# Performance work log

Hardware: AMD Instinct MI355X
Metric: run time of the kernel (lower is better)

The kernel has to match this reference:

```python
import jax, jax.numpy as jnp
import numpy as np

B, A, C, L, NH, SCALE = 1, 5, 64, 4, 8, 2
H = W = 24
S = 2 * C
KS = 5


def layernorm(x, g, b, eps=1e-5):
    m = x.mean(-1, keepdims=True)
    v = ((x - m) ** 2).mean(-1, keepdims=True)
    return (x - m) * jax.lax.rsqrt(v + eps) * g + b


def pe_1d(n, d):
    # PositionEncoding: temperature**(2*(i//2)/d), sin of even cols then cos of odd cols
    g = jnp.arange(d, dtype=jnp.float32)
    g = 10000.0 ** (2.0 * jnp.floor(g / 2.0) / d)
    p = jnp.arange(n, dtype=jnp.float32)[:, None] / g[None, :]
    return jnp.concatenate([jnp.sin(p[:, 0::2]), jnp.cos(p[:, 1::2])], axis=1)  # [n, d]


def mha(qk, v, in_w, out_w, nh, mask=None):
    # qk, v: [Lq, Bt, D]; torch nn.MultiheadAttention, bias-free, q=k=qk, value=v
    Lq, Bt, D = qk.shape
    dh = D // nh
    wq, wk, wv = jnp.split(in_w, 3, axis=0)
    q = (qk @ wq.T).reshape(Lq, Bt, nh, dh)
    k = (qk @ wk.T).reshape(Lq, Bt, nh, dh)
    vv = (v @ wv.T).reshape(Lq, Bt, nh, dh)
    s = jnp.einsum('lbhd,mbhd->bhlm', q, k) / jnp.sqrt(jnp.float32(dh))
    if mask is not None:
        s = s + mask
    a = jax.nn.softmax(s, axis=-1)
    o = jnp.einsum('bhlm,mbhd->lbhd', a, vv).reshape(Lq, Bt, D)
    return o @ out_w.T


def unfold3x3(x):
    # F.unfold(k=3, pad=1).permute(2,0,1): [N,c,h,w] -> [h*w, N, 9c] (c, kh, kw ordering)
    N, c, h, w = x.shape
    xp = jnp.pad(x, ((0, 0), (0, 0), (1, 1), (1, 1)))
    p = jnp.stack([xp[:, :, i:i + h, j:j + w] for i in range(3) for j in range(3)], axis=2)
    return p.reshape(N, c * 9, h * w).transpose(2, 0, 1)


def conv_hw(x5, w):
    # Conv3d kernel (1,3,3) pad (0,1,1): 2D conv per angular view
    Bc, Ci, Aa, h, w_ = x5.shape
    y = jax.lax.conv_general_dilated(
        x5.transpose(0, 2, 1, 3, 4).reshape(Bc * Aa, Ci, h, w_), w, (1, 1), ((1, 1), (1, 1)),
        dimension_numbers=('NCHW', 'OIHW', 'NCHW'))
    return y.reshape(Bc, Aa, w.shape[0], h, w_).transpose(0, 2, 1, 3, 4)


def window_mask(h, w, k):
    # SpaTrans.gen_mask: additive -inf outside a k x k local window
    kl, kr = k // 2, k - k // 2
    i = jnp.arange(h)
    j = jnp.arange(w)
    mh = (i[None, :] >= i[:, None] - kl) & (i[None, :] < i[:, None] + kr)
    mw = (j[None, :] >= j[:, None] - kl) & (j[None, :] < j[:, None] + kr)
    m = (mh[:, None, :, None] & mw[None, :, None, :]).reshape(h * w, h * w)
    return jnp.where(m, 0.0, -jnp.inf).astype(jnp.float32)


def setup_inputs() -> dict:
    key = jax.random.key(0)
    ks = iter(jax.random.split(key, 64))
    def nrm(shape, s=0.02):
        return jax.random.normal(next(ks), shape, dtype=jnp.float32) * s
    d = {}
    d['lr'] = jax.random.normal(next(ks), (B, 1, A * H, A * W), dtype=jnp.float32)
    Hh, Wh = H * SCALE, W * SCALE
    ch = -1.0 + (2.0 * jnp.arange(Hh, dtype=jnp.float32) + 1.0) / Hh
    cw = -1.0 + (2.0 * jnp.arange(Wh, dtype=jnp.float32) + 1.0) / Wh
    g = jnp.stack(jnp.meshgrid(ch, cw, indexing='ij'), axis=-1).reshape(-1, 2)
    d['coord'] = jnp.broadcast_to(g, (B, Hh * Wh, 2))
    d['conv0_w'] = nrm((C, 1, 3, 3), 0.1)
    d['convi_w'] = nrm((3, C, C, 3, 3), 0.05)
    d['ang_ln_g'] = jnp.ones((L, C)); d['ang_ln_b'] = jnp.zeros((L, C))
    d['ang_in'] = nrm((L, 3 * C, C)); d['ang_out'] = nrm((L, C, C))
    d['ang_ff_g'] = jnp.ones((L, C)); d['ang_ff_b'] = jnp.zeros((L, C))
    d['ang_w1'] = nrm((L, 2 * C, C)); d['ang_w2'] = nrm((L, C, 2 * C))
    d['spa_mlp'] = nrm((L, S, 9 * C))
    d['spa_ln_g'] = jnp.ones((L, S)); d['spa_ln_b'] = jnp.zeros((L, S))
    d['spa_in'] = nrm((L, 3 * S, S)); d['spa_out'] = nrm((L, S, S))
    d['spa_ff_g'] = jnp.ones((L, S)); d['spa_ff_b'] = jnp.zeros((L, S))
    d['spa_w1'] = nrm((L, 2 * S, S)); d['spa_w2'] = nrm((L, S, 2 * S))
    d['spa_lin'] = nrm((L, C, S))
    IN = A * A * C + 2 + 2 * A * A
    d['imp_w0'] = nrm((320, IN)); d['imp_b0'] = jnp.zeros((320,))
    d['imp_w1'] = nrm((320, 320)); d['imp_b1'] = jnp.zeros((320,))
    d['imp_w2'] = nrm((3 * A * A, 320)); d['imp_b2'] = jnp.zeros((3 * A * A,))
    return d


def reference(lr, coord, conv0_w, convi_w, ang_ln_g, ang_ln_b, ang_in, ang_out,
              ang_ff_g, ang_ff_b, ang_w1, ang_w2, spa_mlp, spa_ln_g, spa_ln_b,
              spa_in, spa_out, spa_ff_g, spa_ff_b, spa_w1, spa_w2, spa_lin,
              imp_w0, imp_b0, imp_w1, imp_b1, imp_w2, imp_b2):
    Bn = lr.shape[0]
    # 'b c (a1 h) (a2 w) -> b c (a1 a2) h w'
    x = lr.reshape(Bn, 1, A, H, A, W).transpose(0, 1, 2, 4, 3, 5).reshape(Bn, 1, A * A, H, W)
    spa_pe_img = ((pe_1d(H, C)[:, None, :] + pe_1d(W, C)[None, :, :]) * 0.5).transpose(2, 0, 1)[None]  # [1,C,h,w]
    ang_pe = pe_1d(A * A, C)[:, None, :]  # [A^2,1,C]
    buf = conv_hw(x, conv0_w)
    t = buf
    for i in range(3):
        t = jax.nn.leaky_relu(conv_hw(t, convi_w[i]), 0.2)
    buf = t + buf
    mask = window_mask(H, W, KS)
    blk = buf
    for l in range(L):
        # ---- AngTrans: tokens [A^2, B*h*w, C]
        tok = blk.transpose(2, 0, 3, 4, 1).reshape(A * A, Bn * H * W, C)
        tn = layernorm(tok + ang_pe, ang_ln_g[l], ang_ln_b[l])
        tok = mha(tn, tok, ang_in[l], ang_out[l], NH) + tok
        ff = layernorm(tok, ang_ff_g[l], ang_ff_b[l])
        tok = jax.nn.relu(ff @ ang_w1[l].T) @ ang_w2[l].T + tok
        blk = tok.reshape(A * A, Bn, H, W, C).transpose(1, 4, 0, 2, 3)
        # ---- SpaTrans: tokens [h*w, B*A^2, 2C] with local-window mask
        xb = blk.transpose(0, 2, 1, 3, 4).reshape(Bn * A * A, C, H, W)
        tok = unfold3x3(xb) @ spa_mlp[l].T
        pe_tok = unfold3x3(spa_pe_img) @ spa_mlp[l].T
        tn = layernorm(tok + pe_tok, spa_ln_g[l], spa_ln_b[l])
        tok = mha(tn, tok, spa_in[l], spa_out[l], NH, mask) + tok
        ff = layernorm(tok, spa_ff_g[l], spa_ff_b[l])
        tok = jax.nn.relu(ff @ spa_w1[l].T) @ spa_w2[l].T + tok
        t5 = tok.reshape(H, W, Bn, A * A, S).transpose(2, 4, 3, 0, 1)  # b s a h w
        blk = jnp.einsum('os,bsahw->boahw', spa_lin[l], t5)  # 1x1x1 Conv3d
    buf = blk + buf
    # 'b c (a1 a2) h w -> b c (a1 h) (a2 w)'
    feat_lr = buf.reshape(Bn, C, A, A, H, W).transpose(0, 1, 2, 4, 3, 5).reshape(Bn, C, A * H, A * W)
    Hh, Wh = H * SCALE, W * SCALE
    # per-view bilinear upsample (align_corners=False)
    v = feat_lr.reshape(Bn, C, A, H, A, W).transpose(0, 2, 4, 1, 3, 5).reshape(Bn * A * A, C, H, W)
    v = jax.image.resize(v, (Bn * A * A, C, Hh, Wh), method='bilinear')
    feat_hr = v.reshape(Bn, A, A, C, Hh, Wh).transpose(0, 4, 5, 1, 2, 3).reshape(Bn, Hh, Wh, A * A * C)
    # nearest grid_sample of LR cell-center coords -> relative coord
    c_ = jnp.clip(coord + 1e-6, -1 + 1e-6, 1 - 1e-6)
    ih = jnp.clip(jnp.round(((c_[..., 0] + 1) * H - 1) / 2), 0, H - 1)
    iw = jnp.clip(jnp.round(((c_[..., 1] + 1) * W - 1) / 2), 0, W - 1)
    qh = -1.0 + (2.0 * ih + 1.0) / H
    qw = -1.0 + (2.0 * iw + 1.0) / W
    rel = jnp.stack([(coord[..., 0] - qh) * H, (coord[..., 1] - qw) * W], axis=-1).reshape(Bn, Hh, Wh, 2)
    au = 0.5 + jnp.arange(A, dtype=jnp.float32)  # make_coord ranges [0,A]
    ca = jnp.stack(jnp.meshgrid(au, au, indexing='ij'), axis=-1).reshape(-1)
    ca = jnp.broadcast_to(ca, (Bn, Hh, Wh, 2 * A * A))
    inp = jnp.concatenate([feat_hr, rel, ca], axis=-1)
    h0 = jax.nn.relu(inp @ imp_w0.T + imp_b0)
    h1 = jax.nn.relu(h0 @ imp_w1.T + imp_b1)
    o = h1 @ imp_w2.T + imp_b2
    # 'b h w (a1 a2 c) -> b c (a1 h) (a2 w)', c=3
    return o.reshape(Bn, Hh, Wh, A, A, 3).transpose(0, 5, 3, 1, 4, 2).reshape(Bn, 3, A * Hh, A * Wh)
```

## Files before the change

### kernel.cpp

```cpp
#include <hip/hip_runtime.h>
#include <math.h>

typedef short  s16x4 __attribute__((ext_vector_type(4)));
typedef short  s16x8 __attribute__((ext_vector_type(8)));
typedef float  f32x4 __attribute__((ext_vector_type(4)));

static const size_t PE25_  = 0;
static const size_t SPAPE_ = 2048;
static const size_t X_     = 38912;
static const size_t CAV_   = 53312;
static const size_t PETOK_ = 54272;
static const size_t W9C_   = 349184;
static const size_t W9S_   = 459776;
static const size_t BUF_   = 754688;
static const size_t BLK_   = 1676288;
static const size_t ATOK_  = 2597888;
static const size_t TNF_   = 3519488;
static const size_t STOK_  = 4441088;
static const size_t STOK2_ = 6284288;
static const size_t AO_    = 8127488;
static const size_t QKV_   = 9970688;
static const size_t WS_FLOATS = 15500288;
static const size_t T0_ = QKV_ + 2764800;
static const size_t T1_ = T0_ + 921600;
// ... 57 lines not shown
    #pragma unroll
    for (int i = 0; i < 2; ++i) {
      const char* pa = ldsA + (((wr*2 + i)*2 + ks) << 11) + (lane << 4);
      ah[i] = *(const s16x8*)pa;
      al[i] = *(const s16x8*)(pa + 1024);
      const char* pb = ldsB + (((wc*2 + i)*2 + ks) << 11) + (lane << 4);
      bh[i] = *(const s16x8*)pb;
      bl[i] = *(const s16x8*)(pb + 1024);
    }
    #pragma unroll
    for (int i = 0; i < 2; ++i) {
      #pragma unroll
      for (int j = 0; j < 2; ++j) {
        acc[i][j] = __builtin_amdgcn_mfma_f32_16x16x32_bf16(ah[i], bh[j], acc[i][j], 0, 0, 0);
        acc[i][j] = __builtin_amdgcn_mfma_f32_16x16x32_bf16(ah[i], bl[j], acc[i][j], 0, 0, 0);
        acc[i][j] = __builtin_amdgcn_mfma_f32_16x16x32_bf16(al[i], bh[j], acc[i][j], 0, 0, 0);
      }
    }
  }
}

__device__ inline void epilogue(f32x4 acc[2][2], const float* bias, const float* res,
                                float* out, int N, int m0, int n0,
                                int wr, int wc, int lane, int act) {
  int colb = n0 + wc*32 + (lane & 15);
  int rowb = m0 + wr*32 + ((lane >> 4) << 2);
  #pragma unroll
  for (int j = 0; j < 2; ++j) {
    int cc = colb + j*16;
    if (cc >= N) continue;
    float bv = bias ? bias[cc] : 0.f;
    #pragma unroll
    for (int i = 0; i < 2; ++i) {
      #pragma unroll
      for (int r = 0; r < 4; ++r) {
        int rr = rowb + i*16 + r;
        float v = acc[i][j][r] + bv;
        if (act == 1) v = fmaxf(v, 0.f);
        else if (act == 2) v = v > 0.f ? v : 0.2f*v;
        if (res) v += res[(long)rr*N + cc];
        if (act == 3) {
          int hh = rr / 48, ww2 = rr % 48, q = cc / 3, ch = cc % 3;
          out[ch*57600 + ((q/5)*48 + hh)*240 + (q%5)*48 + ww2] = v;
        } else if (act == 4) {
          ((ushort*)out)[(long)rr*N + cc] = f2bf(v);
        } else {
          out[(long)rr*N + cc] = v;
        }
      }
    }
  }
}

template<int K, int LN>
__global__ __launch_bounds__(256) void mgemm3_k(
    const float* __restrict__ A, const float* __restrict__ A2, int nsplit,
    const float* __restrict__ pe, int pe_mode,
    const float* __restrict__ g, const float* __restrict__ bb,
    const float* __restrict__ W, const float* __restrict__ bias,
    const float* __restrict__ res, float* __restrict__ out,
    int N, int act, int Mreal, int Mpad) {
  constexpr int NCH = K / 64;
  __shared__ char Apl[NCH * 16384];
  __shared__ char Bp[16384];
  __shared__ float sw_[4][64][2];
  __shared__ float sf_[64][2];
  int bid = blockIdx.x;
  int m = bid % Mpad, nt = bid / Mpad;
  if (m >= Mreal) return;
  int m0 = m*64, n0 = nt*64;
  int t = threadIdx.x, lane = t & 63, wave = t >> 6;
  int wr = wave >> 1, wc = wave & 1;
  bool use_norm = LN && (n0 < nsplit);

  if (LN && use_norm) {
    f32x4 rv[NCH][4];
    float sA[4], sQ[4];
    #pragma unroll
    for (int i = 0; i < 4; ++i) { sA[i] = 0.f; sQ[i] = 0.f; }
    #pragma unroll
    for (int ch = 0; ch < NCH; ++ch)
      #pragma unroll
      for (int i = 0; i < 4; ++i) {
        int row, kof, wo; slot_decode(i, wave, lane, row, kof, wo);
        int gk = ch*64 + kof;
        f32x4 av = *(const f32x4*)&A[(long)(m0 + row)*K + gk];
        if (pe_mode == 0)      av += *(const f32x4*)&pe[(long)(m0/576)*K + gk];
        else if (pe_mode == 1) av += *(const f32x4*)&pe[(long)(m0%576 + row)*K + gk];
        rv[ch][i] = av;
        #pragma unroll
        for (int e = 0; e < 4; ++e) { sA[i] += av[e]; sQ[i] = fmaf(av[e], av[e], sQ[i]); }
      }
    #pragma unroll
    for (int i = 0; i < 4; ++i) {
      float s = sA[i], q = sQ[i];
      s += __shfl_xor(s, 1, 64);  q += __shfl_xor(q, 1, 64);
      s += __shfl_xor(s, 32, 64); q += __shfl_xor(q, 32, 64);
      if ((lane & 1) == 0 && lane < 32) {
        int row = i*16 + (lane >> 1);
        sw_[wave][row][0] = s; sw_[wave][row][1] = q;
      }
    }
    __syncthreads();
    if (t < 64) {
      float s = sw_[0][t][0] + sw_[1][t][0] + sw_[2][t][0] + sw_[3][t][0];
      float q = sw_[0][t][1] + sw_[1][t][1] + sw_[2][t][1] + sw_[3][t][1];
      float mean = s / K, var = q / K - mean*mean;
      sf_[t][0] = mean; sf_[t][1] = rsqrtf(var + 1e-5f);
    }
    __syncthreads();
    #pragma unroll
    for (int ch = 0; ch < NCH; ++ch)
      #pragma unroll
      for (int i = 0; i < 4; ++i) {
        int row, kof, wo; slot_decode(i, wave, lane, row, kof, wo);
        int gk = ch*64 + kof;
        float mean = sf_[row][0], rstd = sf_[row][1];
        f32x4 gv = *(const f32x4*)&g[gk];
        f32x4 bv = *(const f32x4*)&bb[gk];
        f32x4 nv;
        #pragma unroll
        for (int e = 0; e < 4; ++e) nv[e] = (rv[ch][i][e] - mean)*rstd*gv[e] + bv[e];
        store_split(Apl + ch*16384 + wo, nv);
      }
  } else {
    const float* As = LN ? A2 : A;
    #pragma unroll
    for (int ch = 0; ch < NCH; ++ch)
      #pragma unroll
      for (int i = 0; i < 4; ++i) {
        int row, kof, wo; slot_decode(i, wave, lane, row, kof, wo);
        f32x4 av = *(const f32x4*)&As[(long)(m0 + row)*K + ch*64 + kof];
        store_split(Apl + ch*16384 + wo, av);
      }
  }

  f32x4 pb[4];
  #pragma unroll
  for (int i = 0; i < 4; ++i) {
    int row, kof, wo; slot_decode(i, wave, lane, row, kof, wo);
    int br = n0 + row;
    pb[i] = (br < N) ? *(const f32x4*)&W[(long)br*K + kof] : (f32x4){0.f,0.f,0.f,0.f};
  }
  __syncthreads();
  f32x4 acc[2][2];
  #pragma unroll
  for (int i = 0; i < 2; ++i)
    #pragma unroll
    for (int j = 0; j < 2; ++j) acc[i][j] = (f32x4){0.f,0.f,0.f,0.f};
  for (int ch = 0; ch < NCH; ++ch) {
    #pragma unroll
    for (int i = 0; i < 4; ++i) {
      int row, kof, wo; slot_decode(i, wave, lane, row, kof, wo);
      store_split(Bp + wo, pb[i]);
    }
    __syncthreads();
    if (ch + 1 < NCH) {
      #pragma unroll
      for (int i = 0; i < 4; ++i) {
        int row, kof, wo; slot_decode(i, wave, lane, row, kof, wo);
        int br = n0 + row;
        pb[i] = (br < N) ? *(const f32x4*)&W[(long)br*K + (ch+1)*64 + kof]
                         : (f32x4){0.f,0.f,0.f,0.f};
      }
    }
    mfma_step(Apl + ch*16384, Bp, lane, wr, wc, acc);
    if (ch + 1 < NCH) __syncthreads();
  }
  epilogue(acc, bias, res, out, N, m0, n0, wr, wc, lane, act);
}

__global__ __launch_bounds__(256) void cgemm3_k(
    const float* __restrict__ in, const float* __restrict__ W9, long wstride,
    const float* __restrict__ res, float* __restrict__ out, long ostride,
    int N, int act, int Mreal, int Mpad) {
  __shared__ float halo[144 * 68];
  __shared__ char Ap[16384], Bp[16384];
  int bid = blockIdx.x;
  int m = bid % Mpad, nt = bid / Mpad;
  if (m >= Mreal) return;
  int ly = blockIdx.y;
  W9  += (long)ly * wstride;
  out += (long)ly * ostride;
  int m0 = m*64, n0 = nt*64;
  int a = m0 / 576, off = m0 % 576;
  int h_lo = off/24 - 1, h_hi = (off + 63)/24 + 1;
  int RH = h_hi - h_lo + 1;
  int t = threadIdx.x, lane = t & 63, wave = t >> 6;
  int wr = wave >> 1, wc = wave & 1;
  for (int sidx = t; sidx < RH*24*16; sidx += 256) {
    int tokr = sidx >> 4, c4 = (sidx & 15) << 2;
    int h = h_lo + tokr/24, w = tokr % 24;
    f32x4 v = {0.f,0.f,0.f,0.f};
    if ((unsigned)h < 24u) v = *(const f32x4*)&in[(long)(a*576 + h*24 + w)*64 + c4];
    *(f32x4*)&halo[tokr*68 + c4] = v;
  }
  f32x4 pb[4];
  #pragma unroll
  for (int i = 0; i < 4; ++i) {
    int row, kof, wo; slot_decode(i, wave, lane, row, kof, wo);
    int br = n0 + row;
    pb[i] = (br < N) ? *(const f32x4*)&W9[(long)br*64 + kof] : (f32x4){0.f,0.f,0.f,0.f};
  }
  __syncthreads();
  f32x4 acc[2][2];
  #pragma unroll
  for (int i = 0; i < 2; ++i)
    #pragma unroll
    for (int j = 0; j < 2; ++j) acc[i][j] = (f32x4){0.f,0.f,0.f,0.f};
  for (int ij = 0; ij < 9; ++ij) {
    int di = ij/3 - 1, dj = ij%3 - 1;
    #pragma unroll
    for (int i = 0; i < 4; ++i) {
      int row, kof, wo; slot_decode(i, wave, lane, row, kof, wo);
      int tok = off + row;
      int h2 = tok/24 + di, w2 = tok%24 + dj;
      f32x4 v = {0.f,0.f,0.f,0.f};
      if ((unsigned)h2 < 24u && (unsigned)w2 < 24u)
        v = *(const f32x4*)&halo[((h2 - h_lo)*24 + w2)*68 + kof];
      store_split(Ap + wo, v);
      store_split(Bp + wo, pb[i]);
    }
    __syncthreads();
    if (ij < 8) {
      #pragma unroll
      for (int i = 0; i < 4; ++i) {
        int row, kof, wo; slot_decode(i, wave, lane, row, kof, wo);
        int br = n0 + row;
        pb[i] = (br < N) ? *(const f32x4*)&W9[((long)(ij+1)*N + br)*64 + kof]
                         : (f32x4){0.f,0.f,0.f,0.f};
      }
    }
    mfma_step(Ap, Bp, lane, wr, wc, acc);
    if (ij < 8) __syncthreads();
  }
  epilogue(acc, nullptr, res, out, N, m0, n0, wr, wc, lane, act);
}

__global__ __launch_bounds__(256) void ang_mega_k(
    const ushort* __restrict__ qkv, const float* __restrict__ Wout,
    const float* __restrict__ blkr, const float* __restrict__ g,
    const float* __restrict__ bb, float* __restrict__ atok, float* __restrict__ tnf) {
  int hw = blockIdx.x;
  __shared__ float lq[25*192];
  __shared__ float lao[25*64];
  __shared__ float po[25*68];
  __shared__ float wout[64*65];
  __shared__ float st[25][2];
  int t = threadIdx.x;
  for (int idx = t; idx < 600; idx += 256) {
    int a3 = idx / 24, c8 = (idx % 24) * 8;
    s16x8 r = *(const s16x8*)&qkv[(long)(a3*576 + hw)*192 + c8];
    #pragma unroll
    for (int e = 0; e < 8; ++e) lq[a3*192 + c8 + e] = bf2f((ushort)r[e]);
  }
  for (int idx = t; idx < 4096; idx += 256) {
    int c = idx >> 6, d = idx & 63;
    wout[c*65 + d] = Wout[idx];
  }
  __syncthreads();
  if (t < 200) {
    int l = t / 8, head = t & 7;
    const float* q = lq + l*192 + head*8;
    float s[25]; float mx = -1e30f;
    #pragma unroll
    for (int mm = 0; mm < 25; ++mm) {
      const float* kk = lq + mm*192 + 64 + head*8;
      float acc = 0.f;
      #pragma unroll
      for (int d = 0; d < 8; ++d) acc = fmaf(q[d], kk[d], acc);
      acc *= 0.3535533905932738f;
      s[mm] = acc; mx = fmaxf(mx, acc);
    }
    float sum = 0.f;
    #pragma unroll
    for (int mm = 0; mm < 25; ++mm) { s[mm] = expf(s[mm] - mx); sum += s[mm]; }
    float inv = 1.f / sum;
    #pragma unroll
    for (int d = 0; d < 8; ++d) {
      float acc = 0.f;
      #pragma unroll
      for (int mm = 0; mm < 25; ++mm) acc = fmaf(s[mm], lq[mm*192 + 128 + head*8 + d], acc);
      lao[l*64 + head*8 + d] = acc * inv;
    }
  }
  __syncthreads();
  for (int idx = t; idx < 1600; idx += 256) {
    int tok = idx >> 6, c = idx & 63;
    const float* ar = &lao[tok*64];
    const float* wr = &wout[c*65];
    float accp = 0.f;
    #pragma unroll 16
    for (int d = 0; d < 64; ++d) accp = fmaf(ar[d], wr[d], accp);
    po[tok*68 + c] = accp + blkr[(long)(tok*576 + hw)*64 + c];
  }
  __syncthreads();
  if (t < 25) {
    float s = 0.f, q = 0.f;
    for (int c = 0; c < 64; ++c) { float x = po[t*68 + c]; s += x; q = fmaf(x, x, q); }
    float mean = s / 64.f, var = q / 64.f - mean*mean;
    st[t][0] = mean; st[t][1] = rsqrtf(var + 1e-5f);
  }
  __syncthreads();
  for (int idx = t; idx < 1600; idx += 256) {
    int tok = idx >> 6, c = idx & 63;
    float x = po[tok*68 + c];
    long gidx = (long)(tok*576 + hw)*64 + c;
    atok[gidx] = x;
    tnf[gidx] = (x - st[tok][0]) * st[tok][1] * g[c] + bb[c];
  }
}

__global__ __launch_bounds__(256) void ffn_ang_k(
    const float* __restrict__ tnf, const float* __restrict__ w1,
    const float* __restrict__ w2, float* __restrict__ atok,
    int Mreal, int Mpad) {
  __shared__ char Ap[16384], Bp[16384], Hp[2][16384];
  int bid = blockIdx.x;
  int m = bid % Mpad;
  if (m >= Mreal) return;
  int m0 = m*64;
  int t = threadIdx.x, lane = t & 63, wave = t >> 6;
  int wr = wave >> 1, wc = wave & 1;
  #pragma unroll
  for (int i = 0; i < 4; ++i) {
    int row, kof, wo; slot_decode(i, wave, lane, row, kof, wo);
    f32x4 av = *(const f32x4*)&tnf[(long)(m0 + row)*64 + kof];
    store_split(Ap + wo, av);
  }
  f32x4 pb[4];
  #pragma unroll
  for (int i = 0; i < 4; ++i) {
    int row, kof, wo; slot_decode(i, wave, lane, row, kof, wo);
    pb[i] = *(const f32x4*)&w1[(long)row*64 + kof];
  }
  __syncthreads();
  for (int nt = 0; nt < 2; ++nt) {
    #pragma unroll
    for (int i = 0; i < 4; ++i) {
      int row, kof, wo; slot_decode(i, wave, lane, row, kof, wo);
      store_split(Bp + wo, pb[i]);
    }
    __syncthreads();
    #pragma unroll
    for (int i = 0; i < 4; ++i) {
      int row, kof, wo; slot_decode(i, wave, lane, row, kof, wo);
      pb[i] = (nt == 0) ? *(const f32x4*)&w1[(long)(64 + row)*64 + kof]
                        : *(const f32x4*)&w2[(long)row*128 + kof];
    }
    f32x4 acc[2][2];
    #pragma unroll
    for (int i = 0; i < 2; ++i)
      #pragma unroll
      for (int j = 0; j < 2; ++j) acc[i][j] = (f32x4){0.f,0.f,0.f,0.f};
    mfma_step(Ap, Bp, lane, wr, wc, acc);
    #pragma unroll
    for (int jj = 0; jj < 2; ++jj)
      #pragma unroll
      for (int ii = 0; ii < 2; ++ii)
        #pragma unroll
        for (int r = 0; r < 4; ++r) {
          int rr = wr*32 + ii*16 + ((lane >> 4) << 2) + r;
          int cc = wc*32 + jj*16 + (lane & 15);
          scatter_split(Hp[nt], rr, cc, fmaxf(acc[ii][jj][r], 0.f));
        }
    __syncthreads();
  }
  f32x4 acc2[2][2];
  #pragma unroll
  for (int i = 0; i < 2; ++i)
    #pragma unroll
    for (int j = 0; j < 2; ++j) acc2[i][j] = (f32x4){0.f,0.f,0.f,0.f};
  for (int ch = 0; ch < 2; ++ch) {
    #pragma unroll
    for (int i = 0; i < 4; ++i) {
      int row, kof, wo; slot_decode(i, wave, lane, row, kof, wo);
      store_split(Bp + wo, pb[i]);
    }
    __syncthreads();
    if (ch == 0) {
      #pragma unroll
      for (int i = 0; i < 4; ++i) {
        int row, kof, wo; slot_decode(i, wave, lane, row, kof, wo);
        pb[i] = *(const f32x4*)&w2[(long)row*128 + 64 + kof];
      }
    }
    mfma_step(Hp[ch], Bp, lane, wr, wc, acc2);
    if (ch == 0) __syncthreads();
  }
  epilogue(acc2, nullptr, atok, atok, 64, m0, 0, wr, wc, lane, 0);
}

__global__ __launch_bounds__(256) void megaspa_k(
    const ushort* __restrict__ qkv, const float* __restrict__ stok,
    const float* __restrict__ wout, const float* __restrict__ g,
    const float* __restrict__ bb, const float* __restrict__ w1,
    const float* __restrict__ w2, const float* __restrict__ wlin,
    float* __restrict__ outb, int Mreal, int Mpad) {
  __shared__ char Aop[32768];
  __shared__ char Bp[16384];
  __shared__ char Hp[4][16384];
  __shared__ float Yf[64][132];
  __shared__ float st[64][2];
  int bid = blockIdx.x;
  int m = bid % Mpad;
  if (m >= Mreal) return;
  int m0 = m*64;
  int t = threadIdx.x, lane = t & 63, wave = t >> 6;
  int wr = wave >> 1, wc = wave & 1;
  float* HpF = (float*)Hp;

  for (int idx = t; idx < 2048; idx += 256) {
    *(f32x4*)&HpF[idx*4] =
        *(const f32x4*)&stok[(long)(m0 + (idx >> 5))*128 + ((idx & 31) << 2)];
  }

  #pragma unroll
  for (int task = 0; task < 2; ++task) {
    int tid = t + task*256;
    int rr = tid >> 3, head = tid & 7;
    int x = m0 + rr;
    int hw = x % 576, h = hw / 24, w = hw % 24;
    float qr[16];
    ld_bf16x16(qkv + (long)x*384 + head*16, qr);
    float s[25]; float mx = -1e30f;
    #pragma unroll
    for (int ro = 0; ro < 5; ++ro) {
      int h2 = h + ro - 2;
      s16x8 k0[5], k1[5];
      #pragma unroll
      for (int co = 0; co < 5; ++co) {
        int xt = x + (ro - 2)*24 + (co - 2);
        xt = min(max(xt, 0), 14399);
        const ushort* kp = qkv + (long)xt*384 + 128 + head*16;
        k0[co] = *(const s16x8*)kp;
        k1[co] = *(const s16x8*)(kp + 8);
      }
      #pragma unroll
      for (int co = 0; co < 5; ++co) {
        int w2 = w + co - 2;
        float sc = -1e30f;
        if (h2 >= 0 && h2 < 24 && w2 >= 0 && w2 < 24) {
          sc = 0.f;
          #pragma unroll
          for (int d = 0; d < 8; ++d) sc = fmaf(qr[d], bf2f((ushort)k0[co][d]), sc);
          #pragma unroll
          for (int d = 0; d < 8; ++d) sc = fmaf(qr[8+d], bf2f((ushort)k1[co][d]), sc);
          sc *= 0.25f;
        }
        s[ro*5 + co] = sc; mx = fmaxf(mx, sc);
      }
    }
    float sum = 0.f;
    #pragma unroll
    for (int i = 0; i < 25; ++i) {
      float e = (s[i] > -1e29f) ? expf(s[i] - mx) : 0.f;
      s[i] = e; sum += e;
    }
    float inv = 1.f / sum;
    float acc[16];
    #pragma unroll
    for (int d = 0; d < 16; ++d) acc[d] = 0.f;
    #pragma unroll
    for (int ro = 0; ro < 5; ++ro) {
      s16x8 v0[5], v1[5];
      #pragma unroll
      for (int co = 0; co < 5; ++co) {
        int xt = x + (ro - 2)*24 + (co - 2);
        xt = min(max(xt, 0), 14399);
        const ushort* vp = qkv + (long)xt*384 + 256 + head*16;
        v0[co] = *(const s16x8*)vp;
        v1[co] = *(const s16x8*)(vp + 8);
      }
      #pragma unroll
      for (int co = 0; co < 5; ++co) {
        float sv = s[ro*5 + co];
        #pragma unroll
        for (int d = 0; d < 8; ++d) acc[d] = fmaf(sv, bf2f((ushort)v0[co][d]), acc[d]);
        #pragma unroll
        for (int d = 0; d < 8; ++d) acc[8+d] = fmaf(sv, bf2f((ushort)v1[co][d]), acc[8+d]);
      }
    }
    #pragma unroll
    for (int d = 0; d < 16; ++d) {
      int cc = head*16 + d;
      scatter_split(Aop + (cc >> 6)*16384, rr, cc & 63, acc[d] * inv);
    }
  }

  for (int nt = 0; nt < 2; ++nt) {
    f32x4 acc[2][2];
    #pragma unroll
    for (int i = 0; i < 2; ++i)
      #pragma unroll
      for (int j = 0; j < 2; ++j) acc[i][j] = (f32x4){0.f,0.f,0.f,0.f};
    for (int ch = 0; ch < 2; ++ch) {
      __syncthreads();
      #pragma unroll
      for (int i = 0; i < 4; ++i) {
        int row, kof, wo; slot_decode(i, wave, lane, row, kof, wo);
        f32x4 bv = *(const f32x4*)&wout[(long)(nt*64 + row)*128 + ch*64 + kof];
        store_split(Bp + wo, bv);
      }
      __syncthreads();
      mfma_step(Aop + ch*16384, Bp, lane, wr, wc, acc);
    }
    int colb = nt*64 + wc*32 + (lane & 15);
    int rowb = wr*32 + ((lane >> 4) << 2);
    #pragma unroll
    for (int j = 0; j < 2; ++j)
      #pragma unroll
      for (int i = 0; i < 2; ++i)
        #pragma unroll
        for (int r = 0; r < 4; ++r) {
          int rr = rowb + i*16 + r, cc = colb + j*16;
          Yf[rr][cc] = acc[i][j][r] + HpF[rr*128 + cc];
        }
  }
  __syncthreads();

  {
    int row = t >> 2, q4 = t & 3;
    const float* yr = &Yf[row][q4*32];
    float s = 0.f, sq = 0.f;
    #pragma unroll
    for (int j2 = 0; j2 < 32; ++j2) { float xv = yr[j2]; s += xv; sq = fmaf(xv, xv, sq); }
    s += __shfl_xor(s, 1, 64); sq += __shfl_xor(sq, 1, 64);
    s += __shfl_xor(s, 2, 64); sq += __shfl_xor(sq, 2, 64);
    if (q4 == 0) {
      float mean = s / 128.f, var = sq / 128.f - mean*mean;
      st[row][0] = mean; st[row][1] = rsqrtf(var + 1e-5f);
    }
  }
  __syncthreads();
  #pragma unroll
  for (int ch = 0; ch < 2; ++ch)
    #pragma unroll
    for (int i = 0; i < 4; ++i) {
      int row, kof, wo; slot_decode(i, wave, lane, row, kof, wo);
      int gk = ch*64 + kof;
      f32x4 xv = *(const f32x4*)&Yf[row][gk];
      float mean = st[row][0], rstd = st[row][1];
      f32x4 gv = *(const f32x4*)&g[gk];
      f32x4 bv = *(const f32x4*)&bb[gk];
      f32x4 nv;
      #pragma unroll
      for (int e = 0; e < 4; ++e) nv[e] = (xv[e] - mean)*rstd*gv[e] + bv[e];
      store_split(Aop + ch*16384 + wo, nv);
    }

  for (int nt = 0; nt < 4; ++nt) {
    f32x4 acc[2][2];
    #pragma unroll
    for (int i = 0; i < 2; ++i)
      #pragma unroll
      for (int j = 0; j < 2; ++j) acc[i][j] = (f32x4){0.f,0.f,0.f,0.f};
    for (int ch = 0; ch < 2; ++ch) {
      __syncthreads();
      #pragma unroll
      for (int i = 0; i < 4; ++i) {
        int row, kof, wo; slot_decode(i, wave, lane, row, kof, wo);
        f32x4 bv = *(const f32x4*)&w1[(long)(nt*64 + row)*128 + ch*64 + kof];
        store_split(Bp + wo, bv);
      }
      __syncthreads();
      mfma_step(Aop + ch*16384, Bp, lane, wr, wc, acc);
    }
    #pragma unroll
    for (int jj = 0; jj < 2; ++jj)
      #pragma unroll
      for (int ii = 0; ii < 2; ++ii)
        #pragma unroll
        for (int r = 0; r < 4; ++r) {
          int rr = wr*32 + ii*16 + ((lane >> 4) << 2) + r;
          int cc = wc*32 + jj*16 + (lane & 15);
          scatter_split(Hp[nt], rr, cc, fmaxf(acc[ii][jj][r], 0.f));
        }
  }

  for (int nt2 = 0; nt2 < 2; ++nt2) {
    f32x4 acc2[2][2];
    #pragma unroll
    for (int i = 0; i < 2; ++i)
      #pragma unroll
      for (int j = 0; j < 2; ++j) acc2[i][j] = (f32x4){0.f,0.f,0.f,0.f};
    for (int ch = 0; ch < 4; ++ch) {
      __syncthreads();
      #pragma unroll
      for (int i = 0; i < 4; ++i) {
        int row, kof, wo; slot_decode(i, wave, lane, row, kof, wo);
        f32x4 bv = *(const f32x4*)&w2[(long)(nt2*64 + row)*256 + ch*64 + kof];
        store_split(Bp + wo, bv);
      }
      __syncthreads();
      mfma_step(Hp[ch], Bp, lane, wr, wc, acc2);
    }
    #pragma unroll
    for (int jj = 0; jj < 2; ++jj)
      #pragma unroll
      for (int ii = 0; ii < 2; ++ii)
        #pragma unroll
        for (int r = 0; r < 4; ++r) {
          int rr = wr*32 + ii*16 + ((lane >> 4) << 2) + r;
          int cc = wc*32 + jj*16 + (lane & 15);
          scatter_split(Aop + nt2*16384, rr, cc,
                        acc2[ii][jj][r] + Yf[rr][nt2*64 + cc]);
        }
  }

  f32x4 acc3[2][2];
  #pragma unroll
  for (int i = 0; i < 2; ++i)
    #pragma unroll
    for (int j = 0; j < 2; ++j) acc3[i][j] = (f32x4){0.f,0.f,0.f,0.f};
  for (int ch = 0; ch < 2; ++ch) {
    __syncthreads();
    #pragma unroll
    for (int i = 0; i < 4; ++i) {
      int row, kof, wo; slot_decode(i, wave, lane, row, kof, wo);
      f32x4 bv = *(const f32x4*)&wlin[(long)row*128 + ch*64 + kof];
      store_split(Bp + wo, bv);
    }
    __syncthreads();
    mfma_step(Aop + ch*16384, Bp, lane, wr, wc, acc3);
  }
  epilogue(acc3, nullptr, nullptr, outb, 64, m0, 0, wr, wc, lane, 0);
}

__global__ __launch_bounds__(256) void zgemm3_k(
    const float* __restrict__ buf, const float* __restrict__ blk,
    const float* __restrict__ W0, float* __restrict__ Zp) {
  __shared__ char Ap[16384], Bp[16384];
  int bid = blockIdx.x;
  int m = bid % 16; if (m >= 9) return;
  int nz = bid / 16;
  int n = nz % 5, z = nz / 5;
  int m0 = m*64, n0 = n*64;
  int t = threadIdx.x, lane = t & 63, wave = t >> 6;
  int wr = wave >> 1, wc = wave & 1;
  f32x4 pa[4], pb[4];
  #pragma unroll
  for (int i = 0; i < 4; ++i) {
    int row, kof, wo; slot_decode(i, wave, lane, row, kof, wo);
    long tok = (long)(z*5)*576 + m0 + row;
    pa[i] = *(const f32x4*)&buf[tok*64 + kof];
    pa[i] += *(const f32x4*)&blk[tok*64 + kof];
    pb[i] = *(const f32x4*)&W0[(long)(n0 + row)*1652 + (z*5)*64 + kof];
  }
  f32x4 acc[2][2];
  #pragma unroll
  for (int i = 0; i < 2; ++i)
    #pragma unroll
    for (int j = 0; j < 2; ++j) acc[i][j] = (f32x4){0.f,0.f,0.f,0.f};
  for (int q = 0; q < 5; ++q) {
    #pragma unroll
    for (int i = 0; i < 4; ++i) {
      int row, kof, wo; slot_decode(i, wave, lane, row, kof, wo);
      store_split(Ap + wo, pa[i]);
      store_split(Bp + wo, pb[i]);
    }
    __syncthreads();
    if (q < 4) {
      #pragma unroll
      for (int i = 0; i < 4; ++i) {
        int row, kof, wo; slot_decode(i, wave, lane, row, kof, wo);
        long tok = (long)(z*5 + q + 1)*576 + m0 + row;
        pa[i] = *(const f32x4*)&buf[tok*64 + kof];
        pa[i] += *(const f32x4*)&blk[tok*64 + kof];
        pb[i] = *(const f32x4*)&W0[(long)(n0 + row)*1652 + (z*5 + q + 1)*64 + kof];
      }
    }
    mfma_step(Ap, Bp, lane, wr, wc, acc);
    if (q < 4) __syncthreads();
  }
  epilogue(acc, nullptr, nullptr, Zp + (long)z*184320, 320, m0, n0, wr, wc, lane, 0);
}

__global__ void combine_k(const float* __restrict__ Zp, const float* __restrict__ cav,
                          const float* __restrict__ coord, float* __restrict__ h0out) {
  int gidx = blockIdx.x * 256 + threadIdx.x;
  if (gidx >= 2304 * 320) return;
  int p = gidx / 320, o = gidx % 320;
  int hh = p / 48, ww = p % 48;
  float sh = hh * 0.5f - 0.25f, sw = ww * 0.5f - 0.25f;
  int h0i = (int)floorf(sh); float fh = sh - h0i;
  int w0i = (int)floorf(sw); float fw = sw - w0i;
  int h0c = max(h0i, 0), h1c = min(h0i + 1, 23);
  int w0c = max(w0i, 0), w1c = min(w0i + 1, 23);
  int i00 = (h0c*24 + w0c)*320 + o, i01 = (h0c*24 + w1c)*320 + o;
  int i10 = (h1c*24 + w0c)*320 + o, i11 = (h1c*24 + w1c)*320 + o;
  float z00 = 0.f, z01 = 0.f, z10 = 0.f, z11 = 0.f;
  #pragma unroll
  for (int z = 0; z < 5; ++z) {
    const float* Zz = Zp + (long)z*184320;
    z00 += Zz[i00]; z01 += Zz[i01]; z10 += Zz[i10]; z11 += Zz[i11];
  }
  float v = (1.f-fh)*((1.f-fw)*z00 + fw*z01) + fh*((1.f-fw)*z10 + fw*z11);
  #pragma unroll
  for (int d = 0; d < 2; ++d) {
    float co = coord[p*2 + d];
    float cc = fminf(fmaxf(co + 1e-6f, -1.f + 1e-6f), 1.f - 1e-6f);
    float ix = rintf(((cc + 1.f)*24.f - 1.f)*0.5f);
    ix = fminf(fmaxf(ix, 0.f), 23.f);
    float q = -1.f + (2.f*ix + 1.f)/24.f;
    v = fmaf((co - q)*24.f, cav[320*(d+1) + o], v);
  }
  h0out[gidx] = fmaxf(v + cav[o], 0.f);
}

__device__ inline float pe_val(int pos, int c) {
  int j = c & 31;
  float freq = powf(10000.f, -2.f * (float)j / 64.f);
  float arg = (float)pos * freq;
  return (c < 32) ? sinf(arg) : cosf(arg);
}

__global__ void setup_k(const float* __restrict__ lr, const float* __restrict__ convi_w,
                        const float* __restrict__ spa_mlp,
                        const float* __restrict__ imp_w0, const float* __restrict__ imp_b0,
                        float* pe25, float* spa_pe, float* X, float* w9c, float* w9s,
                        float* cav) {
  int g = blockIdx.x * 256 + threadIdx.x;
  if (g < 1600) { pe25[g] = pe_val(g >> 6, g & 63); return; }
  g -= 1600;
  if (g < 36864) {
    int hw = g >> 6, c = g & 63; int h = hw / 24, w = hw % 24;
    spa_pe[g] = 0.5f * (pe_val(h, c) + pe_val(w, c)); return;
  }
  g -= 36864;
  if (g < 14400) {
    int aa = g / 576, hw = g % 576, h = hw / 24, w = hw % 24;
    X[g] = lr[((aa/5)*24 + h)*120 + (aa%5)*24 + w]; return;
  }
  g -= 14400;
  if (g < 110592) {
    int cv = g / 36864, rem = g % 36864;
    int ij = rem / 4096, oc = rem % 4096;
    int o = oc >> 6, c = oc & 63;
    w9c[g] = convi_w[((long)(cv*64 + o)*64 + c)*9 + ij]; return;
  }
  g -= 110592;
  if (g < 294912) {
    int l = g / 73728, rem = g % 73728;
    int ij = rem / 8192, oc = rem % 8192;
    int o = oc >> 6, c = oc & 63;
    w9s[g] = spa_mlp[((long)(l*128 + o))*576 + c*9 + ij]; return;
  }
  g -= 294912;
// ... 29 lines not shown
  float wv[9];
  #pragma unroll
  for (int q = 0; q < 9; ++q) wv[q] = W[lane*9 + q];
  #pragma unroll
  for (int p = 0; p < 12; ++p) {
    float acc = 0.f;
    #pragma unroll
    for (int i = 0; i < 3; ++i)
      #pragma unroll
      for (int j = 0; j < 3; ++j)
        acc = fmaf(patch[sp][i][p + j], wv[i*3 + j], acc);
    out[(long)(a*576 + h*24 + w0 + p)*64 + lane] = acc;
  }
}

extern "C" void kernel_launch(void* const* d_in, const int* in_sizes, int n_in,
                              void* d_out, int out_size, void* d_ws, size_t ws_size,
                              hipStream_t stream) {
  (void)in_sizes; (void)n_in; (void)out_size;
  if (ws_size < (size_t)WS_FLOATS * 4) return;
  float* ws = (float*)d_ws;

  const float* lr       = (const float*)d_in[0];
  const float* coord    = (const float*)d_in[1];
  const float* conv0_w  = (const float*)d_in[2];
  const float* convi_w  = (const float*)d_in[3];
  const float* ang_ln_g = (const float*)d_in[4];
  const float* ang_ln_b = (const float*)d_in[5];
  const float* ang_in   = (const float*)d_in[6];
  const float* ang_out  = (const float*)d_in[7];
  const float* ang_ff_g = (const float*)d_in[8];
  const float* ang_ff_b = (const float*)d_in[9];
  const float* ang_w1   = (const float*)d_in[10];
  const float* ang_w2   = (const float*)d_in[11];
  const float* spa_mlp  = (const float*)d_in[12];
  const float* spa_ln_g = (const float*)d_in[13];
  const float* spa_ln_b = (const float*)d_in[14];
  const float* spa_in   = (const float*)d_in[15];
  const float* spa_out  = (const float*)d_in[16];
  const float* spa_ff_g = (const float*)d_in[17];
  const float* spa_ff_b = (const float*)d_in[18];
  const float* spa_w1   = (const float*)d_in[19];
  const float* spa_w2   = (const float*)d_in[20];
  const float* spa_lin  = (const float*)d_in[21];
  const float* imp_w0   = (const float*)d_in[22];
  const float* imp_b0   = (const float*)d_in[23];
  const float* imp_w1   = (const float*)d_in[24];
  const float* imp_b1   = (const float*)d_in[25];
  const float* imp_w2   = (const float*)d_in[26];
  const float* imp_b2   = (const float*)d_in[27];

  float* pe25 = ws + PE25_;  float* spa_pe = ws + SPAPE_;  float* X = ws + X_;
  float* cav = ws + CAV_;    float* petok = ws + PETOK_;
  float* w9c = ws + W9C_;    float* w9s = ws + W9S_;
  float* buf = ws + BUF_;    float* blk = ws + BLK_;      float* atok = ws + ATOK_;
  float* tnf = ws + TNF_;    float* stok = ws + STOK_;
  float* qkvf = ws + QKV_;   ushort* qkvh = (ushort*)(ws + QKV_);
  float* t0 = ws + T0_;      float* t1 = ws + T1_;
  float* Zp = ws + ZP_;      float* h0 = ws + H0_;        float* h1 = ws + H1_;

  setup_k<<<1792, 256, 0, stream>>>(lr, convi_w, spa_mlp, imp_w0, imp_b0,
                                    pe25, spa_pe, X, w9c, w9s, cav);
  conv0_k<<<300, 256, 0, stream>>>(X, conv0_w, buf);
  cgemm3_k<<<dim3(232,1), 256, 0, stream>>>(buf, w9c,         0, nullptr, t0,  0, 64, 2, 225, 232);
  cgemm3_k<<<dim3(232,1), 256, 0, stream>>>(t0,  w9c + 36864, 0, nullptr, t1,  0, 64, 2, 225, 232);
  cgemm3_k<<<dim3(232,1), 256, 0, stream>>>(t1,  w9c + 73728, 0, buf,     buf, 0, 64, 2, 225, 232);
  cgemm3_k<<<dim3(32, 4), 256, 0, stream>>>(spa_pe, w9s, 73728, nullptr, petok, 73728,
                                            128, 0, 9, 16);

  for (int l = 0; l < 4; ++l) {
    const float* blkr = (l == 0) ? buf : blk;
    mgemm3_k<64,1><<<696, 256, 0, stream>>>(blkr, blkr, 128, pe25, 0,
        ang_ln_g + l*64, ang_ln_b + l*64, ang_in + l*192*64, nullptr, nullptr,
        qkvf, 192, 4, 225, 232);
    ang_mega_k<<<576, 256, 0, stream>>>(qkvh, ang_out + l*64*64, blkr,
        ang_ff_g + l*64, ang_ff_b + l*64, atok, tnf);
    ffn_ang_k<<<232, 256, 0, stream>>>(tnf, ang_w1 + l*128*64, ang_w2 + l*64*128,
        atok, 225, 232);
    cgemm3_k<<<dim3(464,1), 256, 0, stream>>>(atok, w9s + l*73728, 0, nullptr, stok, 0,
        128, 0, 225, 232);
    mgemm3_k<128,1><<<1392, 256, 0, stream>>>(stok, stok, 256, petok + l*73728, 1,
        spa_ln_g + l*128, spa_ln_b + l*128, spa_in + l*384*128, nullptr, nullptr,
        qkvf, 384, 4, 225, 232);
    megaspa_k<<<232, 256, 0, stream>>>(qkvh, stok, spa_out + l*128*128,
        spa_ff_g + l*128, spa_ff_b + l*128, spa_w1 + l*256*128, spa_w2 + l*128*256,
        spa_lin + l*64*128, blk, 225, 232);
  }

  zgemm3_k<<<400, 256, 0, stream>>>(buf, blk, imp_w0, Zp);
  combine_k<<<2880, 256, 0, stream>>>(Zp, cav, coord, h0);
  mgemm3_k<320,0><<<200, 256, 0, stream>>>(h0, h0, 0, nullptr, -1, nullptr, nullptr,
      imp_w1, imp_b1, nullptr, h1, 320, 1, 36, 40);
  mgemm3_k<320,0><<<80, 256, 0, stream>>>(h1, h1, 0, nullptr, -1, nullptr, nullptr,
      imp_w2, imp_b2, nullptr, (float*)d_out, 75, 3, 36, 40);
}
```

Baseline: 652.4 us.

## Split megaspa kernel across two 256-thread wave groups at 512 threads

The fused spatial-attention/FFN kernel now launches with 512 threads, and its two wave groups each take one 64-column output tile of the out-projection, FFN and norm stages, with double-buffered B and hidden tiles. Shared memory is reorganised: the residual is kept in a single Rf buffer that is accumulated in place, and the FFN hidden layer is computed in two rounds of two 64-wide tiles instead of four stored tiles. This doubles the waves per block to raise parallelism, since only 225 blocks run. In exchange, the final linear projection runs on only half the waves, and the extra threads raise per-block register and LDS pressure. Elsewhere only whitespace changes.

```diff
diff --git a/kernel.cpp b/kernel.cpp
--- a/kernel.cpp
+++ b/kernel.cpp
@@ -163,7 +163,8 @@
     for (int ch = 0; ch < NCH; ++ch)
       #pragma unroll
       for (int i = 0; i < 4; ++i) {
-        int row, kof, wo; slot_decode(i, wave, lane, row, kof, wo);
+        int row, kof, wo;
+        slot_decode(i, wave, lane, row, kof, wo);
         int gk = ch*64 + kof;
         f32x4 av = *(const f32x4*)&A[(long)(m0 + row)*K + gk];
         if (pe_mode == 0)      av += *(const f32x4*)&pe[(long)(m0/576)*K + gk];
@@ -194,7 +195,8 @@
     for (int ch = 0; ch < NCH; ++ch)
       #pragma unroll
       for (int i = 0; i < 4; ++i) {
-        int row, kof, wo; slot_decode(i, wave, lane, row, kof, wo);
+        int row, kof, wo;
+        slot_decode(i, wave, lane, row, kof, wo);
         int gk = ch*64 + kof;
         float mean = sf_[row][0], rstd = sf_[row][1];
         f32x4 gv = *(const f32x4*)&g[gk];
@@ -210,7 +212,8 @@
     for (int ch = 0; ch < NCH; ++ch)
       #pragma unroll
       for (int i = 0; i < 4; ++i) {
-        int row, kof, wo; slot_decode(i, wave, lane, row, kof, wo);
+        int row, kof, wo;
+        slot_decode(i, wave, lane, row, kof, wo);
         f32x4 av = *(const f32x4*)&As[(long)(m0 + row)*K + ch*64 + kof];
         store_split(Apl + ch*16384 + wo, av);
       }
@@ -219,7 +222,8 @@
   f32x4 pb[4];
   #pragma unroll
   for (int i = 0; i < 4; ++i) {
-    int row, kof, wo; slot_decode(i, wave, lane, row, kof, wo);
+    int row, kof, wo;
+    slot_decode(i, wave, lane, row, kof, wo);
     int br = n0 + row;
     pb[i] = (br < N) ? *(const f32x4*)&W[(long)br*K + kof] : (f32x4){0.f,0.f,0.f,0.f};
   }
@@ -232,14 +236,16 @@
   for (int ch = 0; ch < NCH; ++ch) {
     #pragma unroll
     for (int i = 0; i < 4; ++i) {
-      int row, kof, wo; slot_decode(i, wave, lane, row, kof, wo);
+      int row, kof, wo;
+      slot_decode(i, wave, lane, row, kof, wo);
       store_split(Bp + wo, pb[i]);
     }
     __syncthreads();
     if (ch + 1 < NCH) {
       #pragma unroll
       for (int i = 0; i < 4; ++i) {
-        int row, kof, wo; slot_decode(i, wave, lane, row, kof, wo);
+        int row, kof, wo;
+        slot_decode(i, wave, lane, row, kof, wo);
         int br = n0 + row;
         pb[i] = (br < N) ? *(const f32x4*)&W[(long)br*K + (ch+1)*64 + kof]
                          : (f32x4){0.f,0.f,0.f,0.f};
@@ -279,7 +285,8 @@
   f32x4 pb[4];
   #pragma unroll
   for (int i = 0; i < 4; ++i) {
-    int row, kof, wo; slot_decode(i, wave, lane, row, kof, wo);
+    int row, kof, wo;
+    slot_decode(i, wave, lane, row, kof, wo);
     int br = n0 + row;
     pb[i] = (br < N) ? *(const f32x4*)&W9[(long)br*64 + kof] : (f32x4){0.f,0.f,0.f,0.f};
   }
@@ -293,7 +300,8 @@
     int di = ij/3 - 1, dj = ij%3 - 1;
     #pragma unroll
     for (int i = 0; i < 4; ++i) {
-      int row, kof, wo; slot_decode(i, wave, lane, row, kof, wo);
+      int row, kof, wo;
+      slot_decode(i, wave, lane, row, kof, wo);
       int tok = off + row;
       int h2 = tok/24 + di, w2 = tok%24 + dj;
       f32x4 v = {0.f,0.f,0.f,0.f};
@@ -306,7 +314,8 @@
     if (ij < 8) {
       #pragma unroll
       for (int i = 0; i < 4; ++i) {
-        int row, kof, wo; slot_decode(i, wave, lane, row, kof, wo);
+        int row, kof, wo;
+        slot_decode(i, wave, lane, row, kof, wo);
         int br = n0 + row;
         pb[i] = (br < N) ? *(const f32x4*)&W9[((long)(ij+1)*N + br)*64 + kof]
                          : (f32x4){0.f,0.f,0.f,0.f};
@@ -405,27 +414,31 @@
   int wr = wave >> 1, wc = wave & 1;
   #pragma unroll
   for (int i = 0; i < 4; ++i) {
-    int row, kof, wo; slot_decode(i, wave, lane, row, kof, wo);
+    int row, kof, wo;
+    slot_decode(i, wave, lane, row, kof, wo);
     f32x4 av = *(const f32x4*)&tnf[(long)(m0 + row)*64 + kof];
     store_split(Ap + wo, av);
   }
   f32x4 pb[4];
   #pragma unroll
   for (int i = 0; i < 4; ++i) {
-    int row, kof, wo; slot_decode(i, wave, lane, row, kof, wo);
+    int row, kof, wo;
+    slot_decode(i, wave, lane, row, kof, wo);
     pb[i] = *(const f32x4*)&w1[(long)row*64 + kof];
   }
   __syncthreads();
   for (int nt = 0; nt < 2; ++nt) {
     #pragma unroll
     for (int i = 0; i < 4; ++i) {
-      int row, kof, wo; slot_decode(i, wave, lane, row, kof, wo);
+      int row, kof, wo;
+      slot_decode(i, wave, lane, row, kof, wo);
       store_split(Bp + wo, pb[i]);
     }
     __syncthreads();
     #pragma unroll
     for (int i = 0; i < 4; ++i) {
-      int row, kof, wo; slot_decode(i, wave, lane, row, kof, wo);
+      int row, kof, wo;
+      slot_decode(i, wave, lane, row, kof, wo);
       pb[i] = (nt == 0) ? *(const f32x4*)&w1[(long)(64 + row)*64 + kof]
                         : *(const f32x4*)&w2[(long)row*128 + kof];
     }
@@ -455,14 +468,16 @@
   for (int ch = 0; ch < 2; ++ch) {
     #pragma unroll
     for (int i = 0; i < 4; ++i) {
-      int row, kof, wo; slot_decode(i, wave, lane, row, kof, wo);
+      int row, kof, wo;
+      slot_decode(i, wave, lane, row, kof, wo);
       store_split(Bp + wo, pb[i]);
     }
     __syncthreads();
     if (ch == 0) {
       #pragma unroll
       for (int i = 0; i < 4; ++i) {
-        int row, kof, wo; slot_decode(i, wave, lane, row, kof, wo);
+        int row, kof, wo;
+        slot_decode(i, wave, lane, row, kof, wo);
         pb[i] = *(const f32x4*)&w2[(long)row*128 + 64 + kof];
       }
     }
@@ -472,34 +487,33 @@
   epilogue(acc2, nullptr, atok, atok, 64, m0, 0, wr, wc, lane, 0);
 }
 
-__global__ __launch_bounds__(256) void megaspa_k(
+__global__ __launch_bounds__(512) void megaspa_k(
     const ushort* __restrict__ qkv, const float* __restrict__ stok,
     const float* __restrict__ wout, const float* __restrict__ g,
     const float* __restrict__ bb, const float* __restrict__ w1,
     const float* __restrict__ w2, const float* __restrict__ wlin,
     float* __restrict__ outb, int Mreal, int Mpad) {
   __shared__ char Aop[32768];
-  __shared__ char Bp[16384];
-  __shared__ char Hp[4][16384];
-  __shared__ float Yf[64][132];
+  __shared__ char Bp2[2][16384];
+  __shared__ char Hp2[2][16384];
+  __shared__ float Rf[64*132];
   __shared__ float st[64][2];
   int bid = blockIdx.x;
   int m = bid % Mpad;
   if (m >= Mreal) return;
   int m0 = m*64;
   int t = threadIdx.x, lane = t & 63, wave = t >> 6;
-  int wr = wave >> 1, wc = wave & 1;
-  float* HpF = (float*)Hp;
-
-  for (int idx = t; idx < 2048; idx += 256) {
-    *(f32x4*)&HpF[idx*4] =
-        *(const f32x4*)&stok[(long)(m0 + (idx >> 5))*128 + ((idx & 31) << 2)];
-  }
-
-  #pragma unroll
-  for (int task = 0; task < 2; ++task) {
-    int tid = t + task*256;
-    int rr = tid >> 3, head = tid & 7;
+  int wgrp = wave >> 2, w4 = wave & 3;
+  int wr = w4 >> 1, wc = w4 & 1;
+  char* Bp = Bp2[wgrp];
+
+  for (int idx = t; idx < 2048; idx += 512) {
+    int row = idx >> 5, c4 = (idx & 31) << 2;
+    *(f32x4*)&Rf[row*132 + c4] = *(const f32x4*)&stok[(long)(m0 + row)*128 + c4];
+  }
+
+  {
+    int rr = t >> 3, head = t & 7;
     int x = m0 + rr;
     int hw = x % 576, h = hw / 24, w = hw % 24;
     float qr[16];
@@ -519,9 +533,9 @@
       }
       #pragma unroll
       for (int co = 0; co < 5; ++co) {
-        int w2 = w + co - 2;
+        int w2c = w + co - 2;
         float sc = -1e30f;
-        if (h2 >= 0 && h2 < 24 && w2 >= 0 && w2 < 24) {
+        if (h2 >= 0 && h2 < 24 && w2c >= 0 && w2c < 24) {
           sc = 0.f;
           #pragma unroll
           for (int d = 0; d < 8; ++d) sc = fmaf(qr[d], bf2f((ushort)k0[co][d]), sc);
@@ -569,7 +583,8 @@
     }
   }
 
-  for (int nt = 0; nt < 2; ++nt) {
+  {
+    int nt = wgrp;
     f32x4 acc[2][2];
     #pragma unroll
     for (int i = 0; i < 2; ++i)
@@ -579,7 +594,8 @@
       __syncthreads();
       #pragma unroll
       for (int i = 0; i < 4; ++i) {
-        int row, kof, wo; slot_decode(i, wave, lane, row, kof, wo);
+        int row, kof, wo;
+        slot_decode(i, w4, lane, row, kof, wo);
         f32x4 bv = *(const f32x4*)&wout[(long)(nt*64 + row)*128 + ch*64 + kof];
         store_split(Bp + wo, bv);
       }
@@ -595,32 +611,34 @@
         #pragma unroll
         for (int r = 0; r < 4; ++r) {
           int rr = rowb + i*16 + r, cc = colb + j*16;
-          Yf[rr][cc] = acc[i][j][r] + HpF[rr*128 + cc];
+          Rf[rr*132 + cc] += acc[i][j][r];
         }
   }
   __syncthreads();
 
   {
-    int row = t >> 2, q4 = t & 3;
-    const float* yr = &Yf[row][q4*32];
+    int row = t >> 3, q8 = t & 7;
+    const float* yr = &Rf[row*132 + q8*16];
     float s = 0.f, sq = 0.f;
     #pragma unroll
-    for (int j2 = 0; j2 < 32; ++j2) { float xv = yr[j2]; s += xv; sq = fmaf(xv, xv, sq); }
+    for (int j2 = 0; j2 < 16; ++j2) { float xv = yr[j2]; s += xv; sq = fmaf(xv, xv, sq); }
     s += __shfl_xor(s, 1, 64); sq += __shfl_xor(sq, 1, 64);
     s += __shfl_xor(s, 2, 64); sq += __shfl_xor(sq, 2, 64);
-    if (q4 == 0) {
+    s += __shfl_xor(s, 4, 64); sq += __shfl_xor(sq, 4, 64);
+    if (q8 == 0) {
       float mean = s / 128.f, var = sq / 128.f - mean*mean;
       st[row][0] = mean; st[row][1] = rsqrtf(var + 1e-5f);
     }
   }
   __syncthreads();
-  #pragma unroll
-  for (int ch = 0; ch < 2; ++ch)
+  {
+    int ch = wgrp;
     #pragma unroll
     for (int i = 0; i < 4; ++i) {
-      int row, kof, wo; slot_decode(i, wave, lane, row, kof, wo);
+      int row, kof, wo;
+      slot_decode(i, w4, lane, row, kof, wo);
       int gk = ch*64 + kof;
-      f32x4 xv = *(const f32x4*)&Yf[row][gk];
+      f32x4 xv = *(const f32x4*)&Rf[row*132 + gk];
       float mean = st[row][0], rstd = st[row][1];
       f32x4 gv = *(const f32x4*)&g[gk];
       f32x4 bv = *(const f32x4*)&bb[gk];
@@ -629,63 +647,68 @@
       for (int e = 0; e < 4; ++e) nv[e] = (xv[e] - mean)*rstd*gv[e] + bv[e];
       store_split(Aop + ch*16384 + wo, nv);
     }
-
-  for (int nt = 0; nt < 4; ++nt) {
-    f32x4 acc[2][2];
+  }
+
+  f32x4 acc2[2][2];
+  #pragma unroll
+  for (int i = 0; i < 2; ++i)
+    #pragma unroll
+    for (int j = 0; j < 2; ++j) acc2[i][j] = (f32x4){0.f,0.f,0.f,0.f};
+  for (int r = 0; r < 2; ++r) {
+    int nt = 2*r + wgrp;
+    f32x4 accH[2][2];
     #pragma unroll
     for (int i = 0; i < 2; ++i)
       #pragma unroll
-      for (int j = 0; j < 2; ++j) acc[i][j] = (f32x4){0.f,0.f,0.f,0.f};
+      for (int j = 0; j < 2; ++j) accH[i][j] = (f32x4){0.f,0.f,0.f,0.f};
     for (int ch = 0; ch < 2; ++ch) {
       __syncthreads();
       #pragma unroll
       for (int i = 0; i < 4; ++i) {
-        int row, kof, wo; slot_decode(i, wave, lane, row, kof, wo);
+        int row, kof, wo;
+        slot_decode(i, w4, lane, row, kof, wo);
         f32x4 bv = *(const f32x4*)&w1[(long)(nt*64 + row)*128 + ch*64 + kof];
         store_split(Bp + wo, bv);
       }
       __syncthreads();
-      mfma_step(Aop + ch*16384, Bp, lane, wr, wc, acc);
+      mfma_step(Aop + ch*16384, Bp, lane, wr, wc, accH);
     }
     #pragma unroll
     for (int jj = 0; jj < 2; ++jj)
       #pragma unroll
       for (int ii = 0; ii < 2; ++ii)
         #pragma unroll
-        for (int r = 0; r < 4; ++r) {
-          int rr = wr*32 + ii*16 + ((lane >> 4) << 2) + r;
+        for (int rx = 0; rx < 4; ++rx) {
+          int rr = wr*32 + ii*16 + ((lane >> 4) << 2) + rx;
           int cc = wc*32 + jj*16 + (lane & 15);
-          scatter_split(Hp[nt], rr, cc, fmaxf(acc[ii][jj][r], 0.f));
+          scatter_split(Hp2[wgrp], rr, cc, fmaxf(accH[ii][jj][rx], 0.f));
         }
-  }
-
-  for (int nt2 = 0; nt2 < 2; ++nt2) {
-    f32x4 acc2[2][2];
-    #pragma unroll
-    for (int i = 0; i < 2; ++i)
-      #pragma unroll
-      for (int j = 0; j < 2; ++j) acc2[i][j] = (f32x4){0.f,0.f,0.f,0.f};
-    for (int ch = 0; ch < 4; ++ch) {
+    for (int q = 0; q < 2; ++q) {
       __syncthreads();
       #pragma unroll
       for (int i = 0; i < 4; ++i) {
-        int row, kof, wo; slot_decode(i, wave, lane, row, kof, wo);
-        f32x4 bv = *(const f32x4*)&w2[(long)(nt2*64 + row)*256 + ch*64 + kof];
+        int row, kof, wo;
+        slot_decode(i, w4, lane, row, kof, wo);
+        f32x4 bv = *(const f32x4*)&w2[(long)(wgrp*64 + row)*256 + (2*r + q)*64 + kof];
         store_split(Bp + wo, bv);
       }
       __syncthreads();
-      mfma_step(Hp[ch], Bp, lane, wr, wc, acc2);
-    }
+      mfma_step(Hp2[q], Bp, lane, wr, wc, acc2);
+    }
+  }
+  {
+    int colb = wc*32 + (lane & 15);
+    int rowb = wr*32 + ((lane >> 4) << 2);
     #pragma unroll
     for (int jj = 0; jj < 2; ++jj)
       #pragma unroll
       for (int ii = 0; ii < 2; ++ii)
         #pragma unroll
-        for (int r = 0; r < 4; ++r) {
-          int rr = wr*32 + ii*16 + ((lane >> 4) << 2) + r;
-          int cc = wc*32 + jj*16 + (lane & 15);
-          scatter_split(Aop + nt2*16384, rr, cc,
-                        acc2[ii][jj][r] + Yf[rr][nt2*64 + cc]);
+        for (int rx = 0; rx < 4; ++rx) {
+          int rr = rowb + ii*16 + rx;
+          int cc = colb + jj*16;
+          scatter_split(Aop + wgrp*16384, rr, cc,
+                        acc2[ii][jj][rx] + Rf[rr*132 + wgrp*64 + cc]);
         }
   }
 
@@ -696,16 +719,20 @@
     for (int j = 0; j < 2; ++j) acc3[i][j] = (f32x4){0.f,0.f,0.f,0.f};
   for (int ch = 0; ch < 2; ++ch) {
     __syncthreads();
-    #pragma unroll
-    for (int i = 0; i < 4; ++i) {
-      int row, kof, wo; slot_decode(i, wave, lane, row, kof, wo);
-      f32x4 bv = *(const f32x4*)&wlin[(long)row*128 + ch*64 + kof];
-      store_split(Bp + wo, bv);
+    if (wgrp == 0) {
+      #pragma unroll
+      for (int i = 0; i < 4; ++i) {
+        int row, kof, wo;
+        slot_decode(i, w4, lane, row, kof, wo);
+        f32x4 bv = *(const f32x4*)&wlin[(long)row*128 + ch*64 + kof];
+        store_split(Bp2[0] + wo, bv);
+      }
     }
     __syncthreads();
-    mfma_step(Aop + ch*16384, Bp, lane, wr, wc, acc3);
-  }
-  epilogue(acc3, nullptr, nullptr, outb, 64, m0, 0, wr, wc, lane, 0);
+    if (wgrp == 0) mfma_step(Aop + ch*16384, Bp2[0], lane, wr, wc, acc3);
+  }
+  if (wgrp == 0)
+    epilogue(acc3, nullptr, nullptr, outb, 64, m0, 0, wr, wc, lane, 0);
 }
 
 __global__ __launch_bounds__(256) void zgemm3_k(
@@ -722,7 +749,8 @@
   f32x4 pa[4], pb[4];
   #pragma unroll
   for (int i = 0; i < 4; ++i) {
-    int row, kof, wo; slot_decode(i, wave, lane, row, kof, wo);
+    int row, kof, wo;
+    slot_decode(i, wave, lane, row, kof, wo);
     long tok = (long)(z*5)*576 + m0 + row;
     pa[i] = *(const f32x4*)&buf[tok*64 + kof];
     pa[i] += *(const f32x4*)&blk[tok*64 + kof];
@@ -736,7 +764,8 @@
   for (int q = 0; q < 5; ++q) {
     #pragma unroll
     for (int i = 0; i < 4; ++i) {
-      int row, kof, wo; slot_decode(i, wave, lane, row, kof, wo);
+      int row, kof, wo;
+      slot_decode(i, wave, lane, row, kof, wo);
       store_split(Ap + wo, pa[i]);
       store_split(Bp + wo, pb[i]);
     }
@@ -744,7 +773,8 @@
     if (q < 4) {
       #pragma unroll
       for (int i = 0; i < 4; ++i) {
-        int row, kof, wo; slot_decode(i, wave, lane, row, kof, wo);
+        int row, kof, wo;
+        slot_decode(i, wave, lane, row, kof, wo);
         long tok = (long)(z*5 + q + 1)*576 + m0 + row;
         pa[i] = *(const f32x4*)&buf[tok*64 + kof];
         pa[i] += *(const f32x4*)&blk[tok*64 + kof];
@@ -940,7 +970,7 @@
     mgemm3_k<128,1><<<1392, 256, 0, stream>>>(stok, stok, 256, petok + l*73728, 1,
         spa_ln_g + l*128, spa_ln_b + l*128, spa_in + l*384*128, nullptr, nullptr,
         qkvf, 384, 4, 225, 232);
-    megaspa_k<<<232, 256, 0, stream>>>(qkvh, stok, spa_out + l*128*128,
+    megaspa_k<<<232, 512, 0, stream>>>(qkvh, stok, spa_out + l*128*128,
         spa_ff_g + l*128, spa_ff_b + l*128, spa_w1 + l*256*128, spa_w2 + l*128*256,
         spa_lin + l*64*128, blk, 225, 232);
   }
```

Result: faster. 598.5 us (-8.3%).
